# Performance work log

Measured on AMD Instinct MI355X. Metric: run time of the kernel, lower is better.

Reference implementation:

```python
import jax, jax.numpy as jnp
import numpy as np

N, F, H, R, B, L, C, E, NB = 8192, 512, 256, 16, 32, 256, 7, 262144, 30
D = F + H


def setup_inputs() -> dict:
    ks = jax.random.split(jax.random.key(0), 16)
    g = lambda k, shape, fan: jax.random.normal(k, shape, jnp.float32) / np.sqrt(fan)
    return {
        "x": jax.random.normal(ks[0], (N, F), jnp.float32),
        "edge_index": jax.random.randint(ks[1], (2, E), 0, N),
        "edge_norm": jax.random.uniform(ks[2], (E,), jnp.float32),
        "edge_type": jax.random.randint(ks[3], (E,), 0, R),
        "seq_lengths": jnp.full((B,), L, dtype=jnp.int32),
        "umask": jnp.ones((B, L), jnp.float32),
        "nodal_attn": 1,
        "avec": 0,
        "basis": g(ks[4], (NB, F, H), F),
        "comp": g(ks[5], (R, NB), NB),
        "root1": g(ks[6], (F, H), F),
        "bias1": jnp.zeros((H,), jnp.float32),
        "w_rel": g(ks[7], (H, H), H),
        "b_rel": jnp.zeros((H,), jnp.float32),
        "w_root": g(ks[8], (H, H), H),
        "w_att": g(ks[9], (D, D), D),
        "b_att": jnp.zeros((D,), jnp.float32),
        "w_lin": g(ks[10], (D, H), D),
        "b_lin": jnp.zeros((H,), jnp.float32),
        "w_fc": g(ks[11], (H, C), H),
        "b_fc": jnp.zeros((C,), jnp.float32),
    }


def reference(x, edge_index, edge_norm, edge_type, seq_lengths, umask,
              nodal_attn, avec, basis, comp, root1, bias1, w_rel, b_rel,
              w_root, w_att, b_att, w_lin, b_lin, w_fc, b_fc):
    n = x.shape[0]
    r = comp.shape[0]
    src, dst = edge_index[0], edge_index[1]
    # ---- RGCNConv (num_bases basis decomposition, mean aggregation per relation, root + bias)
    W = jnp.einsum('rb,bfh->rfh', comp, basis)             # [R,F,H]
    xw = jnp.einsum('nf,rfh->nrh', x, W)                   # [N,R,H]
    msg = xw[src, edge_type]                               # [E,H] gather per edge
    seg = dst * r + edge_type                              # per (node, relation) segment
    cnt = jax.ops.segment_sum(jnp.ones((msg.shape[0],), msg.dtype), seg, num_segments=n * r)
    msg = msg / jnp.maximum(cnt[seg], 1.0)[:, None]
    out1 = jax.ops.segment_sum(msg, dst, num_segments=n) + x @ root1 + bias1
    # ---- GraphConv (add aggregation): W_rel * sum_j h_j + b_rel + W_root * h_i
    agg2 = jax.ops.segment_sum(out1[src], dst, num_segments=n)
    out2 = agg2 @ w_rel + b_rel + out1 @ w_root
    emotions = jnp.concatenate([x, out2], axis=-1)          # [N, F+H]
    if int(nodal_attn):
        seq = np.asarray(seq_lengths)                       # static conversation lengths
        starts = np.concatenate([[0], np.cumsum(seq)[:-1]])
        lmax = int(seq.max())
        rows = [jnp.pad(jax.lax.dynamic_slice_in_dim(emotions, int(s), int(l)),
                        ((0, lmax - int(l)), (0, 0)))
                for s, l in zip(starts, seq)]
        M = jnp.stack(rows, 0).transpose(1, 0, 2)           # [L, B, D]
        mask = umask                                        # [B, L]
        # MatchingAttention 'general2', vectorized over all timesteps t
        X = M @ w_att + b_att                               # transform(x_t) for every t: [L,B,D]
        Mm = M * mask.T[:, :, None]                         # mask memory over seq dim
        scores = jnp.einsum('tbd,sbd->tbs', X, Mm) * mask[None]
        a = jax.nn.softmax(jnp.tanh(scores), axis=-1) * mask[None]
        a = a / jnp.sum(a, axis=-1, keepdims=True)
        att = jnp.einsum('tbs,sbd->tbd', a, M)              # [L,B,D]
        hidden = jax.nn.relu(att @ w_lin + b_lin)
    else:
        hidden = jax.nn.relu(emotions @ w_lin + b_lin)
    # dropout is identity in eval mode
    logits = hidden @ w_fc + b_fc
    if int(avec):
        return logits
    return jax.nn.log_softmax(logits, axis=1)  # faithful: torch uses dim=1
```

## Files before the change

kernel.cpp:

```cpp
#include <hip/hip_runtime.h>
#include <hip/hip_bf16.h>

#define NN 8192
#define FF 512
#define HH 256
#define RR 16
#define BB 32
#define LL 256
#define CC 7
#define EE 262144
#define NBASE 30
#define DD 768

constexpr int FLAG_BIAS = 1, FLAG_RELU = 4, FLAG_TANH = 8,
              FLAG_SPLITOUT = 16, FLAG_TAILOUT = 32, FLAG_TAIL2 = 64;

typedef __attribute__((ext_vector_type(8))) short bf16x8;
typedef __attribute__((ext_vector_type(4))) float f32x4;

__global__ __launch_bounds__(256) void detect_dtype(const unsigned short* __restrict__ xs,
                                                    int* __restrict__ flag) {
  __shared__ int red[256];
  int cnt = 0;
  for (int i = threadIdx.x * 2; i < 8192; i += 512) {
    unsigned short u = xs[i];
    int e = (u >> 7) & 0xFF;
    if (e >= 0xC0) cnt++;
  }
  red[threadIdx.x] = cnt;
  __syncthreads();
  for (int s = 128; s > 0; s >>= 1) {
    if (threadIdx.x < s) red[threadIdx.x] += red[threadIdx.x + s];
    __syncthreads();
  }
  if (threadIdx.x == 0) flag[0] = (red[0] > 16) ? 1 : 0;
}

struct PSeg {
  const void* src;
  float* dst;
  __hip_bfloat16* hi;
  __hip_bfloat16* lo;
  __hip_bfloat16* hi2;
  __hip_bfloat16* lo2;
  long n;
  int R, C, ld, off;
  int type;
  int zero;
};
struct PTable {
  PSeg seg[16];
  int count;
  long total;
};

__global__ __launch_bounds__(256) void prep_all(PTable t, const int* __restrict__ flag) {
  const int fp32 = flag[0];
  for (long i = (long)blockIdx.x * 256 + threadIdx.x; i < t.total;
       i += (long)gridDim.x * 256) {
    long off = i;
    int s = 0;
    while (off >= t.seg[s].n) { off -= t.seg[s].n; s++; }
    const PSeg& sg = t.seg[s];
    if (sg.type == 0) {
      float v = 0.f;
      if (!sg.zero)
        v = fp32 ? ((const float*)sg.src)[off]
                 : __bfloat162float(((const __hip_bfloat16*)sg.src)[off]);
      if (sg.dst) sg.dst[off] = v;
      if (sg.hi) {
        __hip_bfloat16 h = __float2bfloat16(v);
        __hip_bfloat16 l = __float2bfloat16(v - __bfloat162float(h));
        sg.hi[off] = h;
        sg.lo[off] = l;
        if (sg.hi2) {
          long d2 = (off >> 9) * DD + (off & 511);
          sg.hi2[d2] = h;
          sg.lo2[d2] = l;
        }
      }
    } else {
      int r = (int)(off % sg.R), c = (int)(off / sg.R);
      float v = fp32 ? ((const float*)sg.src)[(long)r * sg.C + c]
                     : __bfloat162float(((const __hip_bfloat16*)sg.src)[(long)r * sg.C + c]);
      __hip_bfloat16 h = __float2bfloat16(v);
      long d = (long)c * sg.ld + sg.off + r;
      sg.hi[d] = h;
      sg.lo[d] = __float2bfloat16(v - __bfloat162float(h));
    }
  }
}

__global__ __launch_bounds__(256) void wt_gemm(
    const float* __restrict__ basis, const float* __restrict__ comp,
    float* __restrict__ wt_nat) {
  __shared__ float cs[RR * NBASE];
  int tid = threadIdx.x;
  for (int i = tid; i < RR * NBASE; i += 256) cs[i] = comp[i];
  __syncthreads();
  long col = (long)blockIdx.x * 256 + tid;
  float acc[RR] = {};
  for (int b = 0; b < NBASE; ++b) {
    float v = basis[(long)b * 131072 + col];
#pragma unroll
    for (int r = 0; r < RR; ++r) acc[r] += cs[r * NBASE + b] * v;
  }
#pragma unroll
  for (int r = 0; r < RR; ++r) wt_nat[(long)r * 131072 + col] = acc[r];
}

__global__ __launch_bounds__(256) void wt_transpose(
    const float* __restrict__ wt_nat,
    __hip_bfloat16* __restrict__ hi, __hip_bfloat16* __restrict__ lo) {
  __shared__ float t[32][33];
  const int r = blockIdx.z;
  const int f0 = blockIdx.y * 32, h0 = blockIdx.x * 32;
  const int c = threadIdx.x & 31, rw = threadIdx.x >> 5;
  const float* src = wt_nat + ((long)r * 512 + f0) * 256 + h0;
#pragma unroll
  for (int i = 0; i < 4; ++i)
    t[rw + i * 8][c] = src[(long)(rw + i * 8) * 256 + c];
  __syncthreads();
#pragma unroll
  for (int i = 0; i < 4; ++i) {
    int hh = rw + i * 8;
    float v = t[c][hh];
    long orow = (long)(r * 256 + h0 + hh) * 512 + f0 + c;
    __hip_bfloat16 hv = __float2bfloat16(v);
    hi[orow] = hv;
    lo[orow] = __float2bfloat16(v - __bfloat162float(hv));
  }
}

__device__ __forceinline__ void gload_lds16(const void* g, void* l) {
  __builtin_amdgcn_global_load_lds(
      (const __attribute__((address_space(1))) unsigned int*)g,
      (__attribute__((address_space(3))) unsigned int*)l, 16, 0, 0);
}

__global__ __launch_bounds__(256, 3) void mfma_dual(
    const __hip_bfloat16* __restrict__ A, const __hip_bfloat16* __restrict__ Alo,
    const __hip_bfloat16* __restrict__ Bt, const __hip_bfloat16* __restrict__ Btlo,
    const float* __restrict__ bias, float* __restrict__ C, float* __restrict__ Ct,
    __hip_bfloat16* __restrict__ Chi, __hip_bfloat16* __restrict__ Clo,
    __hip_bfloat16* __restrict__ Chi2, __hip_bfloat16* __restrict__ Clo2,
    int K, int ldc, long sA, long sB, long sC, int flags) {
  __shared__ __hip_bfloat16 Ah[128 * 32];
  __shared__ __hip_bfloat16 Bh[128 * 32];
  __shared__ __hip_bfloat16 Al[128 * 32];
  __shared__ __hip_bfloat16 Bl[128 * 32];
  const int tid = threadIdx.x;
  const int w = tid >> 6, lane = tid & 63;
  const long z = blockIdx.z;
  const long row0 = (long)blockIdx.y * 128, col0 = (long)blockIdx.x * 128;
  const int wm = w & 1, wn = w >> 1;
  const int srow0 = (w * 128 + lane) >> 2;
  const int srow1 = (w * 128 + 64 + lane) >> 2;
  const int kch = (lane & 3) * 8;
  const int fr = lane & 15, q = lane >> 4;
  const bool hasAlo = (Alo != nullptr);
  const __hip_bfloat16* Az = A + z * sA;
  const __hip_bfloat16* Alz = hasAlo ? (Alo + z * sA) : nullptr;
  const __hip_bfloat16* Bz = Bt + z * sB;
  const __hip_bfloat16* Blz = Btlo + z * sB;
  const long aoff0 = (row0 + srow0) * K + kch, aoff1 = (row0 + srow1) * K + kch;
  const long boff0 = (col0 + srow0) * K + kch, boff1 = (col0 + srow1) * K + kch;
  f32x4 acc[4][4] = {};
  for (int k0 = 0; k0 < K; k0 += 32) {
    gload_lds16(Az + aoff0 + k0, Ah + w * 1024);
    gload_lds16(Az + aoff1 + k0, Ah + w * 1024 + 512);
    gload_lds16(Bz + boff0 + k0, Bh + w * 1024);
    gload_lds16(Bz + boff1 + k0, Bh + w * 1024 + 512);
    gload_lds16(Blz + boff0 + k0, Bl + w * 1024);
    gload_lds16(Blz + boff1 + k0, Bl + w * 1024 + 512);
    if (hasAlo) {
      gload_lds16(Alz + aoff0 + k0, Al + w * 1024);
      gload_lds16(Alz + aoff1 + k0, Al + w * 1024 + 512);
    }
    __syncthreads();
    bf16x8 ah[4], bh[4], bl[4];
#pragma unroll
    for (int i = 0; i < 4; ++i) {
      ah[i] = *(const bf16x8*)&Ah[(wm * 64 + i * 16 + fr) * 32 + q * 8];
      bh[i] = *(const bf16x8*)&Bh[(wn * 64 + i * 16 + fr) * 32 + q * 8];
      bl[i] = *(const bf16x8*)&Bl[(wn * 64 + i * 16 + fr) * 32 + q * 8];
    }
#pragma unroll
    for (int i = 0; i < 4; ++i)
#pragma unroll
      for (int j = 0; j < 4; ++j) {
        acc[i][j] = __builtin_amdgcn_mfma_f32_16x16x32_bf16(ah[i], bh[j], acc[i][j], 0, 0, 0);
        acc[i][j] = __builtin_amdgcn_mfma_f32_16x16x32_bf16(ah[i], bl[j], acc[i][j], 0, 0, 0);
      }
    if (hasAlo) {
      bf16x8 al[4];
#pragma unroll
      for (int i = 0; i < 4; ++i)
        al[i] = *(const bf16x8*)&Al[(wm * 64 + i * 16 + fr) * 32 + q * 8];
#pragma unroll
      for (int i = 0; i < 4; ++i)
#pragma unroll
        for (int j = 0; j < 4; ++j)
          acc[i][j] = __builtin_amdgcn_mfma_f32_16x16x32_bf16(al[i], bh[j], acc[i][j], 0, 0, 0);
    }
    __syncthreads();
  }
  const int cr = (lane >> 4) * 4, cc = lane & 15;
  float* Cz = C ? (C + z * sC) : nullptr;
  __hip_bfloat16* Chz = Chi ? (Chi + z * sC) : nullptr;
  __hip_bfloat16* Clz = Clo ? (Clo + z * sC) : nullptr;
#pragma unroll
  for (int i = 0; i < 4; ++i) {
    long rbase = row0 + wm * 64 + i * 16 + cr;
#pragma unroll
    for (int j = 0; j < 4; ++j) {
      long col = col0 + wn * 64 + j * 16 + cc;
      float bv = (flags & FLAG_BIAS) ? bias[col] : 0.f;
#pragma unroll
      for (int r = 0; r < 4; ++r) {
        float v = acc[i][j][r] + bv;
        if (flags & FLAG_RELU) v = fmaxf(v, 0.f);
        if (flags & FLAG_TANH) v = tanhf(v);
        long row = rbase + r;
        if ((flags & FLAG_TAIL2) && col >= 768) {
          long off2 = (row >> 8) * 65536 + (col - 768) * 256 + (row & 255);
          __hip_bfloat16 hv = __float2bfloat16(v);
          Chi2[off2] = hv;
          Clo2[off2] = __float2bfloat16(v - __bfloat162float(hv));
        } else if (flags & FLAG_SPLITOUT) {
          long off = row * ldc + col;
          __hip_bfloat16 hv = __float2bfloat16(v);
          Chz[off] = hv;
          Clz[off] = __float2bfloat16(v - __bfloat162float(hv));
        } else if ((flags & FLAG_TAILOUT) && col >= 4096) {
          Ct[row * 256 + (col - 4096)] = v;
        } else {
          Cz[row * ldc + col] = v;
        }
      }
    }
  }
}

__global__ __launch_bounds__(256) void mfma_b64(
    const __hip_bfloat16* __restrict__ A, const __hip_bfloat16* __restrict__ Alo,
    const __hip_bfloat16* __restrict__ Bt, const __hip_bfloat16* __restrict__ Btlo,
    const float* __restrict__ bias, float* __restrict__ C,
    int K, int ldc, long sA, long sB, long sC, int flags) {
  __shared__ __hip_bfloat16 Ah[64 * 32];
  __shared__ __hip_bfloat16 Bh[64 * 32];
  __shared__ __hip_bfloat16 Al[64 * 32];
  __shared__ __hip_bfloat16 Bl[64 * 32];
  const int tid = threadIdx.x;
  const int w = tid >> 6, lane = tid & 63;
  const long z = blockIdx.z;
  const long row0 = (long)blockIdx.y * 64, col0 = (long)blockIdx.x * 64;
  const int srow = tid >> 2;
  const int kch = (tid & 3) * 8;
  const int fr = lane & 15, q = lane >> 4;
  const bool hasAlo = (Alo != nullptr);
  const __hip_bfloat16* Az = A + z * sA;
  const __hip_bfloat16* Alz = hasAlo ? (Alo + z * sA) : nullptr;
  const __hip_bfloat16* Bz = Bt + z * sB;
  const __hip_bfloat16* Blz = Btlo + z * sB;
  const long aoff = (row0 + srow) * (long)K + kch;
  const long boff = (col0 + srow) * (long)K + kch;
  f32x4 acc[4] = {};
  for (int k0 = 0; k0 < K; k0 += 32) {
    gload_lds16(Az + aoff + k0, Ah + w * 512);
    gload_lds16(Bz + boff + k0, Bh + w * 512);
    gload_lds16(Blz + boff + k0, Bl + w * 512);
    if (hasAlo) gload_lds16(Alz + aoff + k0, Al + w * 512);
    __syncthreads();
    bf16x8 ah, bh[4], bl[4];
    ah = *(const bf16x8*)&Ah[(w * 16 + fr) * 32 + q * 8];
#pragma unroll
    for (int j = 0; j < 4; ++j) {
      bh[j] = *(const bf16x8*)&Bh[(j * 16 + fr) * 32 + q * 8];
      bl[j] = *(const bf16x8*)&Bl[(j * 16 + fr) * 32 + q * 8];
    }
#pragma unroll
    for (int j = 0; j < 4; ++j) {
      acc[j] = __builtin_amdgcn_mfma_f32_16x16x32_bf16(ah, bh[j], acc[j], 0, 0, 0);
      acc[j] = __builtin_amdgcn_mfma_f32_16x16x32_bf16(ah, bl[j], acc[j], 0, 0, 0);
    }
    if (hasAlo) {
      bf16x8 al = *(const bf16x8*)&Al[(w * 16 + fr) * 32 + q * 8];
#pragma unroll
      for (int j = 0; j < 4; ++j)
        acc[j] = __builtin_amdgcn_mfma_f32_16x16x32_bf16(al, bh[j], acc[j], 0, 0, 0);
    }
    __syncthreads();
  }
  const long rbase = row0 + w * 16 + q * 4;
  float* Cz = C + z * sC;
#pragma unroll
  for (int j = 0; j < 4; ++j) {
    long col = col0 + j * 16 + fr;
    float bv = (flags & FLAG_BIAS) ? bias[col] : 0.f;
#pragma unroll
    for (int r = 0; r < 4; ++r) {
      float v = acc[j][r] + bv;
      if (flags & FLAG_RELU) v = fmaxf(v, 0.f);
      if (flags & FLAG_TANH) v = tanhf(v);
      Cz[(rbase + r) * (long)ldc + col] = v;
    }
  }
}

__device__ __forceinline__ void rd4(bf16x8 (&d)[4], const __hip_bfloat16* t,
                                    int rbase, int ro) {
#pragma unroll
  for (int i = 0; i < 4; ++i)
    d[i] = *(const bf16x8*)&t[(rbase + i * 16) * 32 + ro];
}

__device__ __forceinline__ void mm16(f32x4 (&acc)[8][4], int g,
                                     const bf16x8 (&a)[4], const bf16x8 (&b)[4]) {
#pragma unroll
  for (int i = 0; i < 4; ++i)
#pragma unroll
    for (int j = 0; j < 4; ++j)
      acc[g * 4 + i][j] =
          __builtin_amdgcn_mfma_f32_16x16x32_bf16(a[i], b[j], acc[g * 4 + i][j], 0, 0, 0);
}

__global__ __launch_bounds__(512, 2) void mfma_dual8(
    const __hip_bfloat16* __restrict__ A, const __hip_bfloat16* __restrict__ Alo,
    const __hip_bfloat16* __restrict__ Bt, const __hip_bfloat16* __restrict__ Btlo,
    const float* __restrict__ bias, float* __restrict__ C,
    int K, int ldc, int NT) {
  __shared__ __hip_bfloat16 sm[2][4][256 * 32];
  const int tid = threadIdx.x;
  const int w = tid >> 6, lane = tid & 63;
  const int wm = w >> 2, wn = w & 3;
  const int nwg = gridDim.x * gridDim.y;
  const int bid = blockIdx.y * gridDim.x + blockIdx.x;
  const int swz = (bid & 7) * (nwg >> 3) + (bid >> 3);
  const int ty = swz % gridDim.y, tx = swz / gridDim.y;
  const long row0 = (long)ty * 256, col0 = (long)tx * 256;
  const int urow = tid >> 2;
  const int qg = (tid & 3) ^ ((tid >> 3) & 3);
  const long ga0 = (row0 + urow) * (long)K + qg * 8, ga1 = ga0 + 128L * K;
  const long gb0 = (col0 + urow) * (long)K + qg * 8, gb1 = gb0 + 128L * K;
  const int fr = lane & 15, q = lane >> 4;
  const int ro = fr * 32 + ((q ^ ((fr >> 1) & 3)) << 3);
  const int arow = wm * 128, brow = wn * 64;
  const int lw = w * 512;
  f32x4 acc[8][4] = {};

  auto stage = [&](int b, long k) {
    gload_lds16(A + ga0 + k, &sm[b][0][lw]);
    gload_lds16(A + ga1 + k, &sm[b][0][4096 + lw]);
    gload_lds16(Bt + gb0 + k, &sm[b][1][lw]);
    gload_lds16(Bt + gb1 + k, &sm[b][1][4096 + lw]);
    gload_lds16(Alo + ga0 + k, &sm[b][2][lw]);
    gload_lds16(Alo + ga1 + k, &sm[b][2][4096 + lw]);
    gload_lds16(Btlo + gb0 + k, &sm[b][3][lw]);
    gload_lds16(Btlo + gb1 + k, &sm[b][3][4096 + lw]);
  };

  stage(0, 0);
  asm volatile("s_waitcnt vmcnt(0)" ::: "memory");
  __builtin_amdgcn_s_barrier();

  for (int t = 0; t < NT; ++t) {
    const int cur = t & 1, nxt = cur ^ 1;
    if (t + 1 < NT) stage(nxt, (long)(t + 1) << 5);
    const __hip_bfloat16* sA = sm[cur][0];
    const __hip_bfloat16* sB = sm[cur][1];
    const __hip_bfloat16* sAl = sm[cur][2];
    const __hip_bfloat16* sBl = sm[cur][3];
    bf16x8 bh[4], bl[4], a0[4], a1[4];
    rd4(bh, sB, brow, ro);
    rd4(bl, sBl, brow, ro);
    rd4(a0, sA, arow, ro);
    rd4(a1, sA, arow + 64, ro);
    __builtin_amdgcn_s_setprio(1);
    mm16(acc, 0, a0, bh);
    mm16(acc, 1, a1, bh);
    mm16(acc, 0, a0, bl);
    mm16(acc, 1, a1, bl);
    __builtin_amdgcn_s_setprio(0);
    rd4(a0, sAl, arow, ro);
    rd4(a1, sAl, arow + 64, ro);
    __builtin_amdgcn_s_setprio(1);
    mm16(acc, 0, a0, bh);
    mm16(acc, 1, a1, bh);
    __builtin_amdgcn_s_setprio(0);
    asm volatile("s_waitcnt vmcnt(0)" ::: "memory");
    __builtin_amdgcn_s_barrier();
  }

  float* ep = (float*)&sm[0][0][0];
  const int EPLD = 260;
  float bvj[4];
#pragma unroll
  for (int j = 0; j < 4; ++j) bvj[j] = bias[col0 + wn * 64 + j * 16 + fr];
  const int band = tid >> 8, tl = tid & 255;
#pragma unroll
  for (int i = 0; i < 8; ++i) {
    __builtin_amdgcn_s_barrier();
#pragma unroll
    for (int j = 0; j < 4; ++j) {
      int colt = wn * 64 + j * 16 + fr;
#pragma unroll
      for (int r = 0; r < 4; ++r)
        ep[(wm * 16 + q * 4 + r) * EPLD + colt] = acc[i][j][r] + bvj[j];
    }
    __builtin_amdgcn_s_barrier();
#pragma unroll
    for (int s = 0; s < 4; ++s) {
      int idx = s * 256 + tl;
      int rw = idx >> 6, c4 = idx & 63;
      float4 v = *(const float4*)&ep[(band * 16 + rw) * EPLD + c4 * 4];
      long grow = row0 + band * 128 + i * 16 + rw;
      *(float4*)&C[grow * (long)ldc + col0 + c4 * 4] = v;
    }
  }
}

__global__ __launch_bounds__(256) void count_edges(
    const int* __restrict__ ei, const int* __restrict__ et, float* __restrict__ cnt) {
  int e = blockIdx.x * 256 + threadIdx.x;
  if (e < EE) atomicAdd(&cnt[ei[EE + e] * RR + et[e]], 1.0f);
}

__global__ __launch_bounds__(256) void scan_rowptr(
    const float* __restrict__ cntf, int* __restrict__ rowptr, int* __restrict__ fill) {
  __shared__ int part[256];
  int tid = threadIdx.x;
  int base = tid * 32;
  int local[32];
  int s = 0;
  for (int i = 0; i < 32; ++i) {
    local[i] = s;
    const float* c = &cntf[(base + i) * RR];
    int d = 0;
#pragma unroll
    for (int r = 0; r < RR; ++r) d += (int)c[r];
    s += d;
  }
  part[tid] = s;
  __syncthreads();
  for (int off = 1; off < 256; off <<= 1) {
    int v = (tid >= off) ? part[tid - off] : 0;
    __syncthreads();
    part[tid] += v;
    __syncthreads();
  }
  int prev = (tid == 0) ? 0 : part[tid - 1];
  for (int i = 0; i < 32; ++i) rowptr[base + i] = prev + local[i];
  if (tid == 255) rowptr[8192] = part[255];
  for (int i = tid; i < 8192; i += 256) fill[i] = 0;
}

__global__ __launch_bounds__(256) void edge_fill(
    const int* __restrict__ ei, const int* __restrict__ et,
    const int* __restrict__ rowptr, int* __restrict__ fill, int* __restrict__ eidx) {
  int e = blockIdx.x * 256 + threadIdx.x;
  if (e < EE) {
    int dst = ei[EE + e];
    int pos = rowptr[dst] + atomicAdd(&fill[dst], 1);
    eidx[pos] = ei[e] | (et[e] << 16);
  }
}

__global__ __launch_bounds__(256) void rgcn_gather(
    const int* __restrict__ rowptr, const int* __restrict__ eidx,
    const float* __restrict__ cntf, const float* __restrict__ xw,
    float* __restrict__ out1, __hip_bfloat16* __restrict__ a2o1_hi,
    __hip_bfloat16* __restrict__ a2o1_lo) {
  const int dst = blockIdx.x;
  const int tid = threadIdx.x;
  const int w = tid >> 6, lane = tid & 63;
  const int c4 = lane * 4;
  __shared__ float inv[RR];
  __shared__ int se[256];
  __shared__ float part[3][256];
  if (tid < RR) inv[tid] = 1.0f / fmaxf(cntf[dst * RR + tid], 1.0f);
  const int beg = rowptr[dst], end = rowptr[dst + 1];
  float4 a = make_float4(0.f, 0.f, 0.f, 0.f);
  for (int c0 = beg; c0 < end; c0 += 256) {
    int n = min(256, end - c0);
    __syncthreads();
    if (tid < n) se[tid] = eidx[c0 + tid];
    __syncthreads();
    int i = w;
    for (; i + 4 < n; i += 8) {
      int p0 = se[i], p1 = se[i + 4];
      float4 v0 = *(const float4*)&xw[((long)(p0 & 0xFFFF) << 12) + ((p0 >> 16) << 8) + c4];
      float4 v1 = *(const float4*)&xw[((long)(p1 & 0xFFFF) << 12) + ((p1 >> 16) << 8) + c4];
      float s0 = inv[p0 >> 16], s1 = inv[p1 >> 16];
      a.x += v0.x * s0 + v1.x * s1;
      a.y += v0.y * s0 + v1.y * s1;
      a.z += v0.z * s0 + v1.z * s1;
      a.w += v0.w * s0 + v1.w * s1;
    }
    for (; i < n; i += 4) {
      int p0 = se[i];
      float4 v0 = *(const float4*)&xw[((long)(p0 & 0xFFFF) << 12) + ((p0 >> 16) << 8) + c4];
      float s0 = inv[p0 >> 16];
      a.x += v0.x * s0;
      a.y += v0.y * s0;
      a.z += v0.z * s0;
      a.w += v0.w * s0;
    }
  }
  __syncthreads();
  if (w) *(float4*)&part[w - 1][c4] = a;
  __syncthreads();
  if (w == 0) {
    float4 p0 = *(const float4*)&part[0][c4];
    float4 p1 = *(const float4*)&part[1][c4];
    float4 p2 = *(const float4*)&part[2][c4];
    long ob = ((long)dst << 8) + c4;
    float4 o = *(const float4*)&out1[ob];
    float t0 = o.x + a.x + p0.x + p1.x + p2.x;
    float t1 = o.y + a.y + p0.y + p1.y + p2.y;
    float t2 = o.z + a.z + p0.z + p1.z + p2.z;
    float t3 = o.w + a.w + p0.w + p1.w + p2.w;
    *(float4*)&out1[ob] = make_float4(t0, t1, t2, t3);
    __hip_bfloat16 h0 = __float2bfloat16(t0), h1 = __float2bfloat16(t1),
                   h2 = __float2bfloat16(t2), h3 = __float2bfloat16(t3);
    ushort4 hv = {*(unsigned short*)&h0, *(unsigned short*)&h1,
                  *(unsigned short*)&h2, *(unsigned short*)&h3};
    __hip_bfloat16 l0 = __float2bfloat16(t0 - __bfloat162float(h0)),
                   l1 = __float2bfloat16(t1 - __bfloat162float(h1)),
                   l2 = __float2bfloat16(t2 - __bfloat162float(h2)),
                   l3 = __float2bfloat16(t3 - __bfloat162float(h3));
    ushort4 lv = {*(unsigned short*)&l0, *(unsigned short*)&l1,
                  *(unsigned short*)&l2, *(unsigned short*)&l3};
    long d = (long)dst * 512 + 256 + c4;
    *(ushort4*)(a2o1_hi + d) = hv;
    *(ushort4*)(a2o1_lo + d) = lv;
  }
}

__global__ __launch_bounds__(256) void graphconv_gather(
    const int* __restrict__ rowptr, const int* __restrict__ eidx,
    const float* __restrict__ out1, __hip_bfloat16* __restrict__ a2o1_hi,
    __hip_bfloat16* __restrict__ a2o1_lo) {
  const int dst = blockIdx.x;
  const int tid = threadIdx.x;
  const int w = tid >> 6, lane = tid & 63;
  const int c4 = lane * 4;
  __shared__ int se[256];
  __shared__ float part[3][256];
  const int beg = rowptr[dst], end = rowptr[dst + 1];
  float4 a = make_float4(0.f, 0.f, 0.f, 0.f);
  for (int c0 = beg; c0 < end; c0 += 256) {
    int n = min(256, end - c0);
    __syncthreads();
    if (tid < n) se[tid] = eidx[c0 + tid];
    __syncthreads();
    int i = w;
    for (; i + 4 < n; i += 8) {
      float4 v0 = *(const float4*)&out1[((long)(se[i] & 0xFFFF) << 8) + c4];
      float4 v1 = *(const float4*)&out1[((long)(se[i + 4] & 0xFFFF) << 8) + c4];
      a.x += v0.x + v1.x;
      a.y += v0.y + v1.y;
      a.z += v0.z + v1.z;
      a.w += v0.w + v1.w;
    }
    for (; i < n; i += 4) {
      float4 v0 = *(const float4*)&out1[((long)(se[i] & 0xFFFF) << 8) + c4];
      a.x += v0.x;
      a.y += v0.y;
      a.z += v0.z;
      a.w += v0.w;
    }
  }
  __syncthreads();
  if (w) *(float4*)&part[w - 1][c4] = a;
  __syncthreads();
  if (w == 0) {
    float4 p0 = *(const float4*)&part[0][c4];
    float4 p1 = *(const float4*)&part[1][c4];
    float4 p2 = *(const float4*)&part[2][c4];
    float t0 = a.x + p0.x + p1.x + p2.x;
    float t1 = a.y + p0.y + p1.y + p2.y;
    float t2 = a.z + p0.z + p1.z + p2.z;
    float t3 = a.w + p0.w + p1.w + p2.w;
    __hip_bfloat16 h0 = __float2bfloat16(t0), h1 = __float2bfloat16(t1),
                   h2 = __float2bfloat16(t2), h3 = __float2bfloat16(t3);
    ushort4 hv = {*(unsigned short*)&h0, *(unsigned short*)&h1,
                  *(unsigned short*)&h2, *(unsigned short*)&h3};
    __hip_bfloat16 l0 = __float2bfloat16(t0 - __bfloat162float(h0)),
                   l1 = __float2bfloat16(t1 - __bfloat162float(h1)),
                   l2 = __float2bfloat16(t2 - __bfloat162float(h2)),
                   l3 = __float2bfloat16(t3 - __bfloat162float(h3));
    ushort4 lv = {*(unsigned short*)&l0, *(unsigned short*)&l1,
                  *(unsigned short*)&l2, *(unsigned short*)&l3};
    long d = (long)dst * 512 + c4;
    *(ushort4*)(a2o1_hi + d) = hv;
    *(ushort4*)(a2o1_lo + d) = lv;
  }
}

__global__ __launch_bounds__(256) void softmax256(const float* __restrict__ S,
                                                  __hip_bfloat16* __restrict__ Ab) {
  __shared__ float red[256];
  long row = blockIdx.x;
  const float* p = S + row * 256;
  int t = threadIdx.x;
  float v = p[t];
  red[t] = v;
  __syncthreads();
  for (int s = 128; s > 0; s >>= 1) {
    if (t < s) red[t] = fmaxf(red[t], red[t + s]);
    __syncthreads();
  }
  float m = red[0];
  __syncthreads();
  float e = __expf(v - m);
  red[t] = e;
  __syncthreads();
  for (int s = 128; s > 0; s >>= 1) {
    if (t < s) red[t] += red[t + s];
    __syncthreads();
  }
  Ab[row * 256 + t] = __float2bfloat16(e / red[0]);
}

__global__ __launch_bounds__(256) void logits_lsm(
    const float* __restrict__ hidden, const float* __restrict__ w_fc,
    const float* __restrict__ b_fc, void* __restrict__ out_v,
    const int* __restrict__ flag) {
  __shared__ float wf[256 * 7];
  __shared__ float lg[224];
  __shared__ float corr[7];
  int t = blockIdx.x;
  int tid = threadIdx.x;
  for (int i = tid; i < 256 * 7; i += 256) wf[i] = w_fc[i];
  __syncthreads();
  if (tid < 224) {
    int b = tid / 7, c = tid % 7;
    const float* hr = hidden + ((long)((b << 8) + t) << 8);
    float s = b_fc[c];
    for (int k = 0; k < 256; ++k) s += hr[k] * wf[k * 7 + c];
    lg[tid] = s;
  }
  __syncthreads();
  if (tid < 7) {
    float m = -1e30f;
    for (int b = 0; b < BB; ++b) m = fmaxf(m, lg[b * 7 + tid]);
    float sum = 0.f;
    for (int b = 0; b < BB; ++b) sum += __expf(lg[b * 7 + tid] - m);
    corr[tid] = m + logf(sum);
  }
  __syncthreads();
  if (tid < 224) {
    float v = lg[tid] - corr[tid % 7];
    if (flag[0]) ((float*)out_v)[t * 224 + tid] = v;
    else ((__hip_bfloat16*)out_v)[t * 224 + tid] = __float2bfloat16(v);
  }
}

extern "C" void kernel_launch(void* const* d_in, const int* in_sizes, int n_in,
                              void* d_out, int out_size, void* d_ws, size_t ws_size,
                              hipStream_t stream) {
  const int* ei = (const int*)d_in[1];
  const int* et = (const int*)d_in[3];

  float* ws = (float*)d_ws;
  int* flag = (int*)d_ws;
  float* p = ws + 16;
  auto alloc = [&](long nf) { float* r = p; p += nf; return r; };
  float* w_fc_f = alloc(1792);
  float* b_rel_f = alloc(256);
  float* biasx = alloc(4352);
  float* battx = alloc(1024);
  float* b_lin_f = alloc(256);
  float* b_fc_f = alloc(16);
  __hip_bfloat16* x_hi = (__hip_bfloat16*)alloc(2097152);
  __hip_bfloat16* x_lo = (__hip_bfloat16*)alloc(2097152);
  __hip_bfloat16* wae_hi = (__hip_bfloat16*)alloc(393216);
  __hip_bfloat16* wae_lo = (__hip_bfloat16*)alloc(393216);
  __hip_bfloat16* wrr_hi = (__hip_bfloat16*)alloc(65536);
  __hip_bfloat16* wrr_lo = (__hip_bfloat16*)alloc(65536);
  __hip_bfloat16* wtc_hi = (__hip_bfloat16*)alloc(1114112);
  __hip_bfloat16* wtc_lo = (__hip_bfloat16*)alloc(1114112);
  float* basis_f = alloc(3932160);
  float* comp_f = alloc(512);
  float* xw = alloc(33554432);
  float* cnt = alloc(131072);
  float* out1 = alloc(2097152);
  __hip_bfloat16* a2o1_hi = (__hip_bfloat16*)alloc(2097152);
  __hip_bfloat16* a2o1_lo = (__hip_bfloat16*)alloc(2097152);
  float* hidden = alloc(2097152);
  int* rowptr = (int*)alloc(8208);
  int* fillc = (int*)alloc(8192);
  int* eidx = (int*)alloc(262144);
  float* wt_nat = xw;
  float* em = xw;
  __hip_bfloat16* emwT_hi = (__hip_bfloat16*)(em + 2097152);
  __hip_bfloat16* emwT_lo = (__hip_bfloat16*)(em + 3145728);
  __hip_bfloat16* em_hi = (__hip_bfloat16*)(em + 6291456);
  __hip_bfloat16* em_lo = (__hip_bfloat16*)(em + 9437184);
  __hip_bfloat16* X_hi = (__hip_bfloat16*)(em + 12582912);
  __hip_bfloat16* X_lo = (__hip_bfloat16*)(em + 15728640);
  float* scores = em + 18874368;
  __hip_bfloat16* a_b16 = (__hip_bfloat16*)(em + 20971520);

  detect_dtype<<<1, 256, 0, stream>>>((const unsigned short*)d_in[0], flag);
  PTable T{};
  long tot = 0;
  int ns = 0;
  auto segL = [&](const void* s, float* d, __hip_bfloat16* hi, __hip_bfloat16* lo,
                  __hip_bfloat16* hi2, __hip_bfloat16* lo2, long n, int z) {
    T.seg[ns] = PSeg{s, d, hi, lo, hi2, lo2, n, 0, 0, 0, 0, 0, z};
    ns++; tot += n;
  };
  auto segT = [&](const void* s, __hip_bfloat16* hi, __hip_bfloat16* lo,
                  int R, int C, int ld, int off) {
    T.seg[ns] = PSeg{s, nullptr, hi, lo, nullptr, nullptr, (long)R * C, R, C, ld, off, 1, 0};
    ns++; tot += (long)R * C;
  };
  segL(d_in[0], nullptr, x_hi, x_lo, nullptr, nullptr, NN * FF, 0);
  segL(d_in[8], basis_f, nullptr, nullptr, nullptr, nullptr, NBASE * FF * HH, 0);
  segL(d_in[9], comp_f, nullptr, nullptr, nullptr, nullptr, RR * NBASE, 0);
  segL(d_in[13], b_rel_f, nullptr, nullptr, nullptr, nullptr, HH, 0);
  segL(d_in[16], battx, nullptr, nullptr, nullptr, nullptr, DD, 0);
  segL(nullptr, battx + DD, nullptr, nullptr, nullptr, nullptr, 256, 1);
  segL(d_in[18], b_lin_f, nullptr, nullptr, nullptr, nullptr, HH, 0);
  segL(d_in[19], w_fc_f, nullptr, nullptr, nullptr, nullptr, HH * CC, 0);
  segL(d_in[20], b_fc_f, nullptr, nullptr, nullptr, nullptr, CC, 0);
  segL(nullptr, biasx, nullptr, nullptr, nullptr, nullptr, 4096, 1);
  segL(d_in[11], biasx + 4096, nullptr, nullptr, nullptr, nullptr, HH, 0);
  segT(d_in[15], wae_hi, wae_lo, DD, DD, DD, 0);
  segT(d_in[17], wae_hi + 768 * 768, wae_lo + 768 * 768, DD, HH, DD, 0);
  segT(d_in[10], wtc_hi + 4096 * 512, wtc_lo + 4096 * 512, FF, HH, FF, 0);
  segT(d_in[12], wrr_hi, wrr_lo, HH, HH, 512, 0);
  segT(d_in[14], wrr_hi, wrr_lo, HH, HH, 512, 256);
  T.count = ns;
  T.total = tot;
  prep_all<<<4096, 256, 0, stream>>>(T, flag);

  wt_gemm<<<131072 / 256, 256, 0, stream>>>(basis_f, comp_f, wt_nat);
  wt_transpose<<<dim3(8, 16, 16), 256, 0, stream>>>(wt_nat, wtc_hi, wtc_lo);
  mfma_dual8<<<dim3(8, 32), 512, 0, stream>>>(
      x_hi, x_lo, wtc_hi, wtc_lo, biasx, xw, FF, 4096, FF / 32);
  mfma_dual8<<<dim3(8, 32), 512, 0, stream>>>(
      x_hi, x_lo, wtc_hi + 2048 * 512, wtc_lo + 2048 * 512, biasx + 2048,
      xw + 2048, FF, 4096, FF / 32);
  mfma_b64<<<dim3(4, 128, 1), 256, 0, stream>>>(
      x_hi, x_lo, wtc_hi + 4096 * 512, wtc_lo + 4096 * 512, biasx + 4096,
      out1, FF, HH, 0, 0, 0, FLAG_BIAS);
  hipMemsetAsync(cnt, 0, 131072 * sizeof(float), stream);
  count_edges<<<EE / 256, 256, 0, stream>>>(ei, et, cnt);
  scan_rowptr<<<1, 256, 0, stream>>>(cnt, rowptr, fillc);
  edge_fill<<<EE / 256, 256, 0, stream>>>(ei, et, rowptr, fillc, eidx);
  rgcn_gather<<<NN, 256, 0, stream>>>(rowptr, eidx, cnt, xw, out1, a2o1_hi, a2o1_lo);
  graphconv_gather<<<NN, 256, 0, stream>>>(rowptr, eidx, out1, a2o1_hi, a2o1_lo);
  extern __global__ void copy_xsplit_k(const __hip_bfloat16*, const __hip_bfloat16*,
                                       __hip_bfloat16*, __hip_bfloat16*);
  copy_xsplit_k<<<(NN * FF) / 256, 256, 0, stream>>>(x_hi, x_lo, em_hi, em_lo);
  mfma_dual<<<dim3(2, 64, 1), 256, 0, stream>>>(
      a2o1_hi, a2o1_lo, wrr_hi, wrr_lo, b_rel_f, nullptr, nullptr,
      em_hi + 512, em_lo + 512, nullptr, nullptr, 512, DD, 0, 0, 0,
      FLAG_BIAS | FLAG_SPLITOUT);
  mfma_dual<<<dim3(8, 64, 1), 256, 0, stream>>>(
      em_hi, em_lo, wae_hi, wae_lo, battx, nullptr, nullptr, X_hi, X_lo,
      emwT_hi, emwT_lo, DD, DD, 0, 0, 0, FLAG_BIAS | FLAG_SPLITOUT | FLAG_TAIL2);
  mfma_b64<<<dim3(4, 4, BB), 256, 0, stream>>>(
      X_hi, X_lo, em_hi, em_lo, nullptr, scores, DD, LL,
      (long)LL * DD, (long)LL * DD, (long)LL * LL, FLAG_TANH);
  softmax256<<<BB * LL, 256, 0, stream>>>(scores, a_b16);
  mfma_b64<<<dim3(4, 4, BB), 256, 0, stream>>>(
      a_b16, nullptr, emwT_hi, emwT_lo, b_lin_f, hidden, LL, HH,
      (long)LL * LL, (long)LL * HH, (long)LL * HH, FLAG_BIAS | FLAG_RELU);
  logits_lsm<<<LL, 256, 0, stream>>>(hidden, w_fc_f, b_fc_f, d_out, flag);
}

__global__ __launch_bounds__(256) void copy_xsplit_k(
    const __hip_bfloat16* __restrict__ xh, const __hip_bfloat16* __restrict__ xl,
    __hip_bfloat16* __restrict__ eh, __hip_bfloat16* __restrict__ el) {
  int idx = blockIdx.x * 256 + threadIdx.x;
  int n = idx >> 9, f = idx & 511;
  long d = (long)n * DD + f;
  eh[d] = xh[idx];
  el[d] = xl[idx];
}
```

Baseline: 578.9 us.

## Swizzle LDS tile layout and remap workgroups for XCD locality in MFMA GEMMs

XOR-swizzles the 16-byte k-chunk position inside each LDS row, on both the global-to-LDS load side and the fragment read side, so the bf16x8 fragment reads hit fewer LDS bank conflicts. For non-batched 128x128 launches whose grid height is a multiple of 8, it also remaps block ids so consecutive tiles land on the same XCD, to improve L2 reuse. This adds a little index arithmetic per block, and the swizzle must match exactly between writer and reader to stay correct.

```diff
diff --git a/kernel.cpp b/kernel.cpp
--- a/kernel.cpp
+++ b/kernel.cpp
@@ -152,12 +152,21 @@
   const int tid = threadIdx.x;
   const int w = tid >> 6, lane = tid & 63;
   const long z = blockIdx.z;
-  const long row0 = (long)blockIdx.y * 128, col0 = (long)blockIdx.x * 128;
+  long by = blockIdx.y, bx = blockIdx.x;
+  if (gridDim.z == 1 && (gridDim.y & 7) == 0) {
+    const int nwg = gridDim.x * gridDim.y;
+    const int bid = blockIdx.y * gridDim.x + blockIdx.x;
+    const int swz = (bid & 7) * (nwg >> 3) + (bid >> 3);
+    by = swz / gridDim.x;
+    bx = swz % gridDim.x;
+  }
+  const long row0 = by * 128, col0 = bx * 128;
   const int wm = w & 1, wn = w >> 1;
   const int srow0 = (w * 128 + lane) >> 2;
   const int srow1 = (w * 128 + 64 + lane) >> 2;
-  const int kch = (lane & 3) * 8;
+  const int kch = ((lane & 3) ^ ((lane >> 3) & 3)) * 8;
   const int fr = lane & 15, q = lane >> 4;
+  const int rq = (q ^ ((fr >> 1) & 3)) * 8;
   const bool hasAlo = (Alo != nullptr);
   const __hip_bfloat16* Az = A + z * sA;
   const __hip_bfloat16* Alz = hasAlo ? (Alo + z * sA) : nullptr;
@@ -181,9 +190,9 @@
     bf16x8 ah[4], bh[4], bl[4];
 #pragma unroll
     for (int i = 0; i < 4; ++i) {
-      ah[i] = *(const bf16x8*)&Ah[(wm * 64 + i * 16 + fr) * 32 + q * 8];
-      bh[i] = *(const bf16x8*)&Bh[(wn * 64 + i * 16 + fr) * 32 + q * 8];
-      bl[i] = *(const bf16x8*)&Bl[(wn * 64 + i * 16 + fr) * 32 + q * 8];
+      ah[i] = *(const bf16x8*)&Ah[(wm * 64 + i * 16 + fr) * 32 + rq];
+      bh[i] = *(const bf16x8*)&Bh[(wn * 64 + i * 16 + fr) * 32 + rq];
+      bl[i] = *(const bf16x8*)&Bl[(wn * 64 + i * 16 + fr) * 32 + rq];
     }
 #pragma unroll
     for (int i = 0; i < 4; ++i)
@@ -196,7 +205,7 @@
       bf16x8 al[4];
 #pragma unroll
       for (int i = 0; i < 4; ++i)
-        al[i] = *(const bf16x8*)&Al[(wm * 64 + i * 16 + fr) * 32 + q * 8];
+        al[i] = *(const bf16x8*)&Al[(wm * 64 + i * 16 + fr) * 32 + rq];
 #pragma unroll
       for (int i = 0; i < 4; ++i)
 #pragma unroll
@@ -256,8 +265,9 @@
   const long z = blockIdx.z;
   const long row0 = (long)blockIdx.y * 64, col0 = (long)blockIdx.x * 64;
   const int srow = tid >> 2;
-  const int kch = (tid & 3) * 8;
+  const int kch = ((tid & 3) ^ ((tid >> 3) & 3)) * 8;
   const int fr = lane & 15, q = lane >> 4;
+  const int rq = (q ^ ((fr >> 1) & 3)) * 8;
   const bool hasAlo = (Alo != nullptr);
   const __hip_bfloat16* Az = A + z * sA;
   const __hip_bfloat16* Alz = hasAlo ? (Alo + z * sA) : nullptr;
@@ -273,11 +283,11 @@
     if (hasAlo) gload_lds16(Alz + aoff + k0, Al + w * 512);
     __syncthreads();
     bf16x8 ah, bh[4], bl[4];
-    ah = *(const bf16x8*)&Ah[(w * 16 + fr) * 32 + q * 8];
+    ah = *(const bf16x8*)&Ah[(w * 16 + fr) * 32 + rq];
 #pragma unroll
     for (int j = 0; j < 4; ++j) {
-      bh[j] = *(const bf16x8*)&Bh[(j * 16 + fr) * 32 + q * 8];
-      bl[j] = *(const bf16x8*)&Bl[(j * 16 + fr) * 32 + q * 8];
+      bh[j] = *(const bf16x8*)&Bh[(j * 16 + fr) * 32 + rq];
+      bl[j] = *(const bf16x8*)&Bl[(j * 16 + fr) * 32 + rq];
     }
 #pragma unroll
     for (int j = 0; j < 4; ++j) {
@@ -285,7 +295,7 @@
       acc[j] = __builtin_amdgcn_mfma_f32_16x16x32_bf16(ah, bl[j], acc[j], 0, 0, 0);
     }
     if (hasAlo) {
-      bf16x8 al = *(const bf16x8*)&Al[(w * 16 + fr) * 32 + q * 8];
+      bf16x8 al = *(const bf16x8*)&Al[(w * 16 + fr) * 32 + rq];
 #pragma unroll
       for (int j = 0; j < 4; ++j)
         acc[j] = __builtin_amdgcn_mfma_f32_16x16x32_bf16(al, bh[j], acc[j], 0, 0, 0);
```

Measured after the change: 602.1 us. 1.04x slower.
